# Performance work log

Hardware: AMD Instinct MI355X
Metric: run time of the kernel (lower is better)

The kernel has to match this reference:

```python
import jax, jax.numpy as jnp
import numpy as np

HEADS = 12
D_MODEL = 768
D_K = D_MODEL // HEADS


def setup_inputs() -> dict:
    key = jax.random.key(0)
    ks = jax.random.split(key, 5)
    B, S = 2, 2048
    scale = 1.0 / np.sqrt(D_MODEL)
    return {
        "q": jax.random.normal(ks[0], (B, S, D_MODEL), dtype=jnp.float32),
        "k": jax.random.normal(ks[1], (B, S, D_MODEL), dtype=jnp.float32),
        "v": jax.random.normal(ks[2], (B, S, D_MODEL), dtype=jnp.float32),
        "Wk": jax.random.normal(ks[3], (D_MODEL, D_MODEL), dtype=jnp.float32) * scale,
        "bk": jnp.zeros((D_MODEL,), dtype=jnp.float32),
        "Wo": jax.random.normal(ks[4], (D_MODEL, D_MODEL), dtype=jnp.float32) * scale,
        "bo": jnp.zeros((D_MODEL,), dtype=jnp.float32),
    }


def reference(q, k, v, Wk, bk, Wo, bo):
    B, S, _ = q.shape
    # NOTE: faithful to source bug: q, k, v ALL projected with k_linear.
    def proj(x):
        y = x @ Wk.T + bk                    # [B,S,D]
        return y.reshape(B, -1, HEADS, D_K).transpose(0, 2, 1, 3)  # [B,H,S,Dk]

    qh, kh, vh = proj(q), proj(k), proj(v)
    scores = jnp.einsum('bhsd,bhtd->bhst', qh, kh) / jnp.sqrt(jnp.float32(D_K))
    attn = jax.nn.softmax(scores, axis=-1)   # dropout is identity in eval
    out = jnp.einsum('bhst,bhtd->bhsd', attn, vh)
    concat = out.transpose(0, 2, 1, 3).reshape(B, -1, D_MODEL)
    return concat @ Wo.T + bo
```

## Files before the change

### kernel.cpp

```cpp
#include <hip/hip_runtime.h>
#include <hip/hip_bf16.h>
#include <stddef.h>

#define HEADS 12
#define DM 768
#define DK 64
#define SEQ 2048
#define NB 2
#define WSZ (DM * DM)
#define QSCALE 0.18033688011112043f

typedef __attribute__((ext_vector_type(8))) short short8;
typedef __attribute__((ext_vector_type(4))) float f32x4;

#define MFMA16(A, B, C) __builtin_amdgcn_mfma_f32_16x16x32_bf16((A), (B), (C), 0, 0, 0)

__device__ __forceinline__ unsigned short f2bf(float x) {
  union { float f; unsigned u; } c;
  c.f = x;
  unsigned r = (c.u + 0x7FFFu + ((c.u >> 16) & 1u)) >> 16;
  return (unsigned short)r;
}
__device__ __forceinline__ float bf2f(unsigned short h) {
  union { float f; unsigned u; } c;
  c.u = ((unsigned)h) << 16;
  return c.f;
}

__device__ __forceinline__ void async16(const void* g, void* l) {
  __builtin_amdgcn_global_load_lds(
      (const __attribute__((address_space(1))) void*)g,
      (__attribute__((address_space(3))) void*)l, 16, 0, 0);
}

__device__ __forceinline__ void splitpk(float a, float b, unsigned& hu, unsigned& lu) {
  union { __hip_bfloat162 v; unsigned u; } c;
  c.v = __float22bfloat162_rn(make_float2(a, b));
  hu = c.u;
  const float ra = a - bf2f((unsigned short)(hu & 0xFFFFu));
  const float rb = b - bf2f((unsigned short)(hu >> 16));
  c.v = __float22bfloat162_rn(make_float2(ra, rb));
  lu = c.u;
}
__device__ __forceinline__ unsigned pk2bf(float a, float b) {
  union { __hip_bfloat162 v; unsigned u; } c;
  c.v = __float22bfloat162_rn(make_float2(a, b));
  return c.u;
}


__global__ __launch_bounds__(256) void prep_split(
    const float* __restrict__ q, const float* __restrict__ k,
    const float* __restrict__ v, const float* __restrict__ Wk,
    const float* __restrict__ Wo, unsigned short* __restrict__ xq,
    unsigned short* __restrict__ xk, unsigned short* __restrict__ xv,
    unsigned short* __restrict__ wkh, unsigned short* __restrict__ wkl,
    unsigned short* __restrict__ woh, unsigned short* __restrict__ wol) {
  __shared__ __align__(16) unsigned short Lh[64 * 136];
  __shared__ __align__(16) unsigned short Ll[64 * 136];
  const int tid = threadIdx.x;
  int id = blockIdx.x;
  const float* S;
  unsigned short *H, *L = nullptr;
  int RT, RT16;
  if (id < 1152) {
    S = (id < 384) ? q : (id < 768) ? k : v;
    H = (id < 384) ? xq : (id < 768) ? xk : xv;
    id = id % 384; RT = 64; RT16 = 256;
  } else if (id < 1224) {
    S = Wk; H = wkh; L = wkl; id -= 1152; RT = 12; RT16 = 48;
  } else {
    S = Wo; H = woh; L = wol; id -= 1224; RT = 12; RT16 = 48;
  }
  const int rb = id % RT, kb = id / RT;
  const int mlane = tid >> 4;
  const int klane = (tid & 15) * 8;

#pragma unroll
  for (int rr = 0; rr < 4; ++rr) {
    const int m = rr * 16 + mlane;
    const float* src = &S[(size_t)(rb * 64 + m) * DM + kb * 128 + klane];
    float a[8];
    *(float4*)&a[0] = *(const float4*)&src[0];
    *(float4*)&a[4] = *(const float4*)&src[4];
    if (L) {
      unsigned hu[4], lu[4];
#pragma unroll
      for (int u = 0; u < 4; ++u) splitpk(a[2 * u], a[2 * u + 1], hu[u], lu[u]);
      *(uint4*)&Lh[m * 136 + klane] = *(uint4*)&hu[0];
      *(uint4*)&Ll[m * 136 + klane] = *(uint4*)&lu[0];
    } else {
      unsigned hu[4];
#pragma unroll
      for (int u = 0; u < 4; ++u) hu[u] = pk2bf(a[2 * u], a[2 * u + 1]);
      *(uint4*)&Lh[m * 136 + klane] = *(uint4*)&hu[0];
    }
  }
  __syncthreads();

  const int t = tid >> 4;
  const int ktp = t >> 2, mtp = t & 3;
  const size_t gt = ((size_t)(kb * 4 + ktp) * RT16 + (rb * 4 + mtp)) * 512;
#pragma unroll
  for (int i = 0; i < 4; ++i) {
    const int c = i * 16 + (tid & 15);
    const int lsrc = (mtp * 16 + (tid & 15)) * 136 + ktp * 32 + i * 8;
    *(uint4*)&H[gt + c * 8] = *(uint4*)&Lh[lsrc];
    if (L) *(uint4*)&L[gt + c * 8] = *(uint4*)&Ll[lsrc];
  }
}

__global__ __launch_bounds__(256, 3) void gemm_proj(
    const unsigned short* __restrict__ Xq, const unsigned short* __restrict__ Xk,
    const unsigned short* __restrict__ Xv, const unsigned short* __restrict__ Bh_,
    const unsigned short* __restrict__ Bl_, const float* __restrict__ bias,
    unsigned short* __restrict__ q_h, unsigned short* __restrict__ q_l,
    unsigned short* __restrict__ k_h, unsigned short* __restrict__ vt_h) {
  __shared__ __align__(16) unsigned short Ash[8 * 512];
  __shared__ __align__(16) unsigned short Bsh[6 * 512];
  __shared__ __align__(16) unsigned short Bsl[6 * 512];

  const int tid = threadIdx.x, z = blockIdx.z;
  const unsigned short* __restrict__ A = (z == 0) ? Xq : (z == 1) ? Xk : Xv;
  const int id = blockIdx.x;
  const int mt0 = (id & 31) * 8, nt0 = (id >> 5) * 6;
  const int lane = tid & 63, wv = tid >> 6;
  const int l15 = lane & 15, quad = lane >> 4;
  const int wm = (wv >> 1) * 4, wn = (wv & 1) * 3;
  const int lx = lane * 8;

  f32x4 acc[4][3];
#pragma unroll
  for (int i = 0; i < 4; ++i)
#pragma unroll
    for (int j = 0; j < 3; ++j) acc[i][j] = (f32x4){0.f, 0.f, 0.f, 0.f};

  for (int kt = 0; kt < 24; ++kt) {
    __syncthreads();
    async16(&A[((size_t)kt * 256 + mt0 + wv) * 512 + lx], &Ash[wv * 512]);
    async16(&A[((size_t)kt * 256 + mt0 + wv + 4) * 512 + lx], &Ash[(wv + 4) * 512]);
    async16(&Bh_[((size_t)kt * 48 + nt0 + wv) * 512 + lx], &Bsh[wv * 512]);
    async16(&Bl_[((size_t)kt * 48 + nt0 + wv) * 512 + lx], &Bsl[wv * 512]);
    if (wv < 2)
      async16(&Bh_[((size_t)kt * 48 + nt0 + 4 + wv) * 512 + lx], &Bsh[(4 + wv) * 512]);
    else
      async16(&Bl_[((size_t)kt * 48 + nt0 + 2 + wv) * 512 + lx], &Bsl[(2 + wv) * 512]);
    __syncthreads();

    short8 bh8[3], bl8[3];
#pragma unroll
    for (int nt = 0; nt < 3; ++nt) {
      bh8[nt] = *(const short8*)&Bsh[(wn + nt) * 512 + lx];
      bl8[nt] = *(const short8*)&Bsl[(wn + nt) * 512 + lx];
    }
#pragma unroll
    for (int mt = 0; mt < 4; ++mt) {
      const short8 ah8 = *(const short8*)&Ash[(wm + mt) * 512 + lx];
#pragma unroll
      for (int nt = 0; nt < 3; ++nt) {
        acc[mt][nt] = MFMA16(ah8, bh8[nt], acc[mt][nt]);
        acc[mt][nt] = MFMA16(ah8, bl8[nt], acc[mt][nt]);
      }
    }
  }

#pragma unroll
  for (int mt = 0; mt < 4; ++mt)
#pragma unroll
    for (int nt = 0; nt < 3; ++nt) {
      const int n = (nt0 + wn + nt) * 16 + l15;
      const float bv = bias[n];
      const int hh = n >> 6, dk = n & 63;
#pragma unroll
      for (int j = 0; j < 4; ++j) {
        const int m = (mt0 + wm + mt) * 16 + quad * 4 + j;
        const int b = m >> 11, t = m & 2047;
        const int bh = b * HEADS + hh;
        if (z == 0) {
          const float y = (acc[mt][nt][j] + bv) * QSCALE;
          const unsigned short yh = f2bf(y);
          const int a = (bh * SEQ + t) * DK + dk;
          q_h[a] = yh;
          q_l[a] = f2bf(y - bf2f(yh));
        } else if (z == 1) {
          const int a = bh * 131072 + (dk >> 5) * 65536 + (t >> 4) * 512 +
                        (((dk & 31) >> 3) * 16 + (t & 15)) * 8 + (dk & 7);
          k_h[a] = f2bf(acc[mt][nt][j] + bv);
        } else {
          const int a = bh * 131072 + (t >> 5) * 2048 + (dk >> 4) * 512 +
                        (((t & 31) >> 3) * 16 + (dk & 15)) * 8 + (t & 7);
          vt_h[a] = f2bf(acc[mt][nt][j] + bv);
        }
      }
    }
}

__global__ __launch_bounds__(256, 2) void gemm_out(
    const unsigned short* __restrict__ Ah_, const unsigned short* __restrict__ Al_,
    const unsigned short* __restrict__ Bh_, const unsigned short* __restrict__ Bl_,
    const float* __restrict__ bias, float* __restrict__ outF) {
  __shared__ __align__(16) unsigned short Ash[4 * 512];
  __shared__ __align__(16) unsigned short Asl[4 * 512];
  __shared__ __align__(16) unsigned short Bsh[6 * 512];
  __shared__ __align__(16) unsigned short Bsl[6 * 512];

  const int tid = threadIdx.x, id = blockIdx.x;
  const int mt0 = (id & 63) * 4, nt0 = (id >> 6) * 6;
  const int lane = tid & 63, wv = tid >> 6;
  const int l15 = lane & 15, quad = lane >> 4;
  const int wm = (wv >> 1) * 2, wn = (wv & 1) * 3;
  const int lx = lane * 8;

  f32x4 acc[2][3];
#pragma unroll
  for (int i = 0; i < 2; ++i)
#pragma unroll
    for (int j = 0; j < 3; ++j) acc[i][j] = (f32x4){0.f, 0.f, 0.f, 0.f};

  for (int kt = 0; kt < 24; ++kt) {
    __syncthreads();
    async16(&Ah_[((size_t)kt * 256 + mt0 + wv) * 512 + lx], &Ash[wv * 512]);
    async16(&Al_[((size_t)kt * 256 + mt0 + wv) * 512 + lx], &Asl[wv * 512]);
    async16(&Bh_[((size_t)kt * 48 + nt0 + wv) * 512 + lx], &Bsh[wv * 512]);
    async16(&Bl_[((size_t)kt * 48 + nt0 + wv) * 512 + lx], &Bsl[wv * 512]);
    if (wv < 2)
      async16(&Bh_[((size_t)kt * 48 + nt0 + 4 + wv) * 512 + lx], &Bsh[(4 + wv) * 512]);
    else
      async16(&Bl_[((size_t)kt * 48 + nt0 + 2 + wv) * 512 + lx], &Bsl[(2 + wv) * 512]);
    __syncthreads();

    short8 bh8[3], bl8[3];
#pragma unroll
    for (int nt = 0; nt < 3; ++nt) {
      bh8[nt] = *(const short8*)&Bsh[(wn + nt) * 512 + lx];
      bl8[nt] = *(const short8*)&Bsl[(wn + nt) * 512 + lx];
    }
#pragma unroll
    for (int mt = 0; mt < 2; ++mt) {
      const short8 ah8 = *(const short8*)&Ash[(wm + mt) * 512 + lx];
      const short8 al8 = *(const short8*)&Asl[(wm + mt) * 512 + lx];
#pragma unroll
      for (int nt = 0; nt < 3; ++nt) {
        acc[mt][nt] = MFMA16(ah8, bh8[nt], acc[mt][nt]);
        acc[mt][nt] = MFMA16(al8, bh8[nt], acc[mt][nt]);
        acc[mt][nt] = MFMA16(ah8, bl8[nt], acc[mt][nt]);
      }
    }
  }

#pragma unroll
  for (int mt = 0; mt < 2; ++mt)
#pragma unroll
    for (int nt = 0; nt < 3; ++nt) {
      const int n = (nt0 + wn + nt) * 16 + l15;
      const float bv = bias[n];
#pragma unroll
      for (int j = 0; j < 4; ++j) {
        const int m = (mt0 + wm + mt) * 16 + quad * 4 + j;
        outF[(size_t)m * DM + n] = acc[mt][nt][j] + bv;
      }
    }
}

__global__ __launch_bounds__(256, 3) void attn_mfma(
    const unsigned short* __restrict__ q_h, const unsigned short* __restrict__ q_l,
    const unsigned short* __restrict__ k_h, const unsigned short* __restrict__ vt_h,
    unsigned short* __restrict__ cch, unsigned short* __restrict__ ccl) {
  __shared__ __align__(16) unsigned short Ks[8 * 512];
  __shared__ __align__(16) unsigned short Vs[8 * 512];
  __shared__ __align__(16) unsigned short Ps[4 * 1024];
  __shared__ float Osh[64 * 68];
  __shared__ float Lred[4][2][16];

  const int tid = threadIdx.x, lane = tid & 63, wv = tid >> 6;
  const int l15 = lane & 15, quad = lane >> 4;
  const int qh = wv & 1, th = wv >> 1;
  const int id = blockIdx.x;
  const int bh = id % 24, q0 = (id / 24) << 6;
  const int lx = lane * 8;

  short8 Qf[2][2][2];
#pragma unroll
  for (int qt = 0; qt < 2; ++qt)
#pragma unroll
    for (int ks = 0; ks < 2; ++ks) {
      const int off =
          (bh * SEQ + q0 + qh * 32 + qt * 16 + l15) * DK + ks * 32 + quad * 8;
      Qf[qt][ks][0] = *(const short8*)&q_h[off];
      Qf[qt][ks][1] = *(const short8*)&q_l[off];
    }

  f32x4 O[2][4];
#pragma unroll
  for (int i = 0; i < 2; ++i)
#pragma unroll
    for (int j = 0; j < 4; ++j) O[i][j] = (f32x4){0.f, 0.f, 0.f, 0.f};
  float lsum[2] = {0.f, 0.f};

  const size_t kbase = (size_t)bh * 131072;
  const size_t vbase = (size_t)bh * 131072;

  for (int t0 = 0; t0 < SEQ; t0 += 64) {
    __syncthreads();
    async16(&k_h[kbase + ((size_t)(t0 >> 4) + wv) * 512 + lx], &Ks[wv * 512]);
    async16(&k_h[kbase + 65536 + ((size_t)(t0 >> 4) + wv) * 512 + lx],
            &Ks[(4 + wv) * 512]);
    async16(&vt_h[vbase + (size_t)(t0 >> 5) * 2048 + wv * 512 + lx],
            &Vs[wv * 512]);
    async16(&vt_h[vbase + ((size_t)(t0 >> 5) + 1) * 2048 + wv * 512 + lx],
            &Vs[(4 + wv) * 512]);
    __syncthreads();

    f32x4 St[2][2];
#pragma unroll
    for (int i = 0; i < 2; ++i)
#pragma unroll
      for (int j = 0; j < 2; ++j) St[i][j] = (f32x4){0.f, 0.f, 0.f, 0.f};
#pragma unroll
    for (int ks = 0; ks < 2; ++ks)
#pragma unroll
      for (int tt = 0; tt < 2; ++tt) {
        const short8 kh8 = *(const short8*)&Ks[(ks * 4 + th * 2 + tt) * 512 + lx];
#pragma unroll
        for (int qt = 0; qt < 2; ++qt) {
          St[tt][qt] = MFMA16(kh8, Qf[qt][ks][0], St[tt][qt]);
          St[tt][qt] = MFMA16(kh8, Qf[qt][ks][1], St[tt][qt]);
        }
      }

#pragma unroll
    for (int tt = 0; tt < 2; ++tt)
#pragma unroll
      for (int qt = 0; qt < 2; ++qt) {
        const float p0 = __builtin_amdgcn_exp2f(fminf(St[tt][qt][0], 40.f));
        const float p1 = __builtin_amdgcn_exp2f(fminf(St[tt][qt][1], 40.f));
        const float p2 = __builtin_amdgcn_exp2f(fminf(St[tt][qt][2], 40.f));
        const float p3 = __builtin_amdgcn_exp2f(fminf(St[tt][qt][3], 40.f));
        lsum[qt] += (p0 + p1) + (p2 + p3);
        unsigned pk[2];
        pk[0] = pk2bf(p0, p1);
        pk[1] = pk2bf(p2, p3);
        *(uint2*)&Ps[wv * 1024 + qt * 512 +
                     ((2 * tt + (quad >> 1)) * 16 + l15) * 8 + (quad & 1) * 4] =
            *(uint2*)&pk[0];
      }
    asm volatile("s_waitcnt lgkmcnt(0)" ::: "memory");

    short8 pf[2];
#pragma unroll
    for (int qt = 0; qt < 2; ++qt)
      pf[qt] = *(const short8*)&Ps[wv * 1024 + qt * 512 + lx];
#pragma unroll
    for (int nt = 0; nt < 4; ++nt) {
      const short8 vh8 = *(const short8*)&Vs[(th * 4 + nt) * 512 + lx];
      O[0][nt] = MFMA16(pf[0], vh8, O[0][nt]);
      O[1][nt] = MFMA16(pf[1], vh8, O[1][nt]);
    }
  }

#pragma unroll
  for (int qt = 0; qt < 2; ++qt) {
    float l = lsum[qt];
    l += __shfl_xor(l, 16);
    l += __shfl_xor(l, 32);
    if (quad == 0) Lred[wv][qt][l15] = l;
  }
  __syncthreads();
  if (th == 1) {
#pragma unroll
    for (int qt = 0; qt < 2; ++qt)
#pragma unroll
      for (int nt = 0; nt < 4; ++nt)
#pragma unroll
        for (int j = 0; j < 4; ++j)
          Osh[(qh * 32 + qt * 16 + quad * 4 + j) * 68 + nt * 16 + l15] =
              O[qt][nt][j];
  }
  __syncthreads();
  if (th == 0) {
    const int b = bh / HEADS, hh = bh % HEADS;
#pragma unroll
    for (int qt = 0; qt < 2; ++qt)
#pragma unroll
      for (int j = 0; j < 4; ++j) {
        const int qloc = qh * 32 + qt * 16 + quad * 4 + j;
        const float inv = 1.0f / (Lred[wv][qt][quad * 4 + j] +
                                  Lred[wv + 2][qt][quad * 4 + j]);
        const int m = b * SEQ + q0 + qloc;
#pragma unroll
        for (int nt = 0; nt < 4; ++nt) {
          const float y = (O[qt][nt][j] + Osh[qloc * 68 + nt * 16 + l15]) * inv;
          const int kk = hh * 64 + nt * 16 + l15;
          const int a = ((kk >> 5) * 256 + (m >> 4)) * 512 +
                        (((kk & 31) >> 3) * 16 + (m & 15)) * 8 + (kk & 7);
          const unsigned short yh = f2bf(y);
          cch[a] = yh;
          ccl[a] = f2bf(y - bf2f(yh));
        }
      }
  }
}

extern "C" void kernel_launch(void* const* d_in, const int* in_sizes, int n_in,
                              void* d_out, int out_size, void* d_ws,
                              size_t ws_size, hipStream_t stream) {
  const float* q = (const float*)d_in[0];
  const float* k = (const float*)d_in[1];
  const float* v = (const float*)d_in[2];
  const float* Wk = (const float*)d_in[3];
  const float* bk = (const float*)d_in[4];
  const float* Wo = (const float*)d_in[5];
  const float* bo = (const float*)d_in[6];
  float* out = (float*)d_out;

  const size_t SZ = (size_t)NB * SEQ * DM;
  unsigned short* ws16 = (unsigned short*)d_ws;
  unsigned short* xq = ws16;
  unsigned short* xk = ws16 + SZ;
  unsigned short* xv = ws16 + 2 * SZ;
  unsigned short* cch = xq;
  unsigned short* ccl = xk;
  unsigned short* qp_h = ws16 + 3 * SZ;
  unsigned short* qp_l = ws16 + 4 * SZ;
  unsigned short* kp = ws16 + 5 * SZ;
  unsigned short* vtp = ws16 + 6 * SZ;
  unsigned short* wkh = ws16 + 7 * SZ;
  unsigned short* wkl = wkh + WSZ;
  unsigned short* woh = wkl + WSZ;
  unsigned short* wol = woh + WSZ;

  prep_split<<<dim3(1296), 256, 0, stream>>>(q, k, v, Wk, Wo, xq, xk, xv, wkh,
                                             wkl, woh, wol);
  gemm_proj<<<dim3(256, 1, 3), 256, 0, stream>>>(xq, xk, xv, wkh, wkl, bk,
                                                 qp_h, qp_l, kp, vtp);
  attn_mfma<<<dim3(768), 256, 0, stream>>>(qp_h, qp_l, kp, vtp, cch, ccl);
  gemm_out<<<dim3(512), 256, 0, stream>>>(cch, ccl, woh, wol, bo, out);
}
```

Before: 206.0 us.

## Halve attention query tile to 32 rows and alias LDS buffers for occupancy

```diff
diff --git a/kernel.cpp b/kernel.cpp
--- a/kernel.cpp
+++ b/kernel.cpp
@@ -262,40 +262,37 @@
     }
 }
 
-__global__ __launch_bounds__(256, 3) void attn_mfma(
+__global__ __launch_bounds__(256, 6) void attn_mfma(
     const unsigned short* __restrict__ q_h, const unsigned short* __restrict__ q_l,
     const unsigned short* __restrict__ k_h, const unsigned short* __restrict__ vt_h,
     unsigned short* __restrict__ cch, unsigned short* __restrict__ ccl) {
-  __shared__ __align__(16) unsigned short Ks[8 * 512];
-  __shared__ __align__(16) unsigned short Vs[8 * 512];
-  __shared__ __align__(16) unsigned short Ps[4 * 1024];
-  __shared__ float Osh[64 * 68];
-  __shared__ float Lred[4][2][16];
+  __shared__ __align__(16) unsigned char pool[16384];
+  unsigned short* const Ks = (unsigned short*)pool;
+  unsigned short* const Vs = (unsigned short*)(pool + 8192);
+  float* const Osh = (float*)pool;
+  __shared__ __align__(16) unsigned short Ps[4 * 512];
+  __shared__ float Lred[4][16];
 
   const int tid = threadIdx.x, lane = tid & 63, wv = tid >> 6;
   const int l15 = lane & 15, quad = lane >> 4;
   const int qh = wv & 1, th = wv >> 1;
   const int id = blockIdx.x;
-  const int bh = id % 24, q0 = (id / 24) << 6;
+  const int bh = id % 24, q0 = (id / 24) << 5;
   const int lx = lane * 8;
 
-  short8 Qf[2][2][2];
-#pragma unroll
-  for (int qt = 0; qt < 2; ++qt)
-#pragma unroll
-    for (int ks = 0; ks < 2; ++ks) {
-      const int off =
-          (bh * SEQ + q0 + qh * 32 + qt * 16 + l15) * DK + ks * 32 + quad * 8;
-      Qf[qt][ks][0] = *(const short8*)&q_h[off];
-      Qf[qt][ks][1] = *(const short8*)&q_l[off];
-    }
-
-  f32x4 O[2][4];
-#pragma unroll
-  for (int i = 0; i < 2; ++i)
-#pragma unroll
-    for (int j = 0; j < 4; ++j) O[i][j] = (f32x4){0.f, 0.f, 0.f, 0.f};
-  float lsum[2] = {0.f, 0.f};
+  short8 Qf[2][2];
+#pragma unroll
+  for (int ks = 0; ks < 2; ++ks) {
+    const int off =
+        (bh * SEQ + q0 + qh * 16 + l15) * DK + ks * 32 + quad * 8;
+    Qf[ks][0] = *(const short8*)&q_h[off];
+    Qf[ks][1] = *(const short8*)&q_l[off];
+  }
+
+  f32x4 O[4];
+#pragma unroll
+  for (int j = 0; j < 4; ++j) O[j] = (f32x4){0.f, 0.f, 0.f, 0.f};
+  float lsum = 0.f;
 
   const size_t kbase = (size_t)bh * 131072;
   const size_t vbase = (size_t)bh * 131072;
@@ -311,93 +308,74 @@
             &Vs[(4 + wv) * 512]);
     __syncthreads();
 
-    f32x4 St[2][2];
-#pragma unroll
-    for (int i = 0; i < 2; ++i)
-#pragma unroll
-      for (int j = 0; j < 2; ++j) St[i][j] = (f32x4){0.f, 0.f, 0.f, 0.f};
+    f32x4 St[2];
+#pragma unroll
+    for (int i = 0; i < 2; ++i) St[i] = (f32x4){0.f, 0.f, 0.f, 0.f};
 #pragma unroll
     for (int ks = 0; ks < 2; ++ks)
 #pragma unroll
       for (int tt = 0; tt < 2; ++tt) {
         const short8 kh8 = *(const short8*)&Ks[(ks * 4 + th * 2 + tt) * 512 + lx];
-#pragma unroll
-        for (int qt = 0; qt < 2; ++qt) {
-          St[tt][qt] = MFMA16(kh8, Qf[qt][ks][0], St[tt][qt]);
-          St[tt][qt] = MFMA16(kh8, Qf[qt][ks][1], St[tt][qt]);
-        }
-      }
-
-#pragma unroll
-    for (int tt = 0; tt < 2; ++tt)
-#pragma unroll
-      for (int qt = 0; qt < 2; ++qt) {
-        const float p0 = __builtin_amdgcn_exp2f(fminf(St[tt][qt][0], 40.f));
-        const float p1 = __builtin_amdgcn_exp2f(fminf(St[tt][qt][1], 40.f));
-        const float p2 = __builtin_amdgcn_exp2f(fminf(St[tt][qt][2], 40.f));
-        const float p3 = __builtin_amdgcn_exp2f(fminf(St[tt][qt][3], 40.f));
-        lsum[qt] += (p0 + p1) + (p2 + p3);
-        unsigned pk[2];
-        pk[0] = pk2bf(p0, p1);
-        pk[1] = pk2bf(p2, p3);
-        *(uint2*)&Ps[wv * 1024 + qt * 512 +
-                     ((2 * tt + (quad >> 1)) * 16 + l15) * 8 + (quad & 1) * 4] =
-            *(uint2*)&pk[0];
-      }
+        St[tt] = MFMA16(kh8, Qf[ks][0], St[tt]);
+        St[tt] = MFMA16(kh8, Qf[ks][1], St[tt]);
+      }
+
+#pragma unroll
+    for (int tt = 0; tt < 2; ++tt) {
+      const float p0 = __builtin_amdgcn_exp2f(fminf(St[tt][0], 40.f));
+      const float p1 = __builtin_amdgcn_exp2f(fminf(St[tt][1], 40.f));
+      const float p2 = __builtin_amdgcn_exp2f(fminf(St[tt][2], 40.f));
+      const float p3 = __builtin_amdgcn_exp2f(fminf(St[tt][3], 40.f));
+      lsum += (p0 + p1) + (p2 + p3);
+      unsigned pk[2];
+      pk[0] = pk2bf(p0, p1);
+      pk[1] = pk2bf(p2, p3);
+      *(uint2*)&Ps[wv * 512 +
+                   ((2 * tt + (quad >> 1)) * 16 + l15) * 8 + (quad & 1) * 4] =
+          *(uint2*)&pk[0];
+    }
     asm volatile("s_waitcnt lgkmcnt(0)" ::: "memory");
 
-    short8 pf[2];
-#pragma unroll
-    for (int qt = 0; qt < 2; ++qt)
-      pf[qt] = *(const short8*)&Ps[wv * 1024 + qt * 512 + lx];
+    const short8 pf = *(const short8*)&Ps[wv * 512 + lx];
 #pragma unroll
     for (int nt = 0; nt < 4; ++nt) {
       const short8 vh8 = *(const short8*)&Vs[(th * 4 + nt) * 512 + lx];
-      O[0][nt] = MFMA16(pf[0], vh8, O[0][nt]);
-      O[1][nt] = MFMA16(pf[1], vh8, O[1][nt]);
-    }
-  }
-
-#pragma unroll
-  for (int qt = 0; qt < 2; ++qt) {
-    float l = lsum[qt];
-    l += __shfl_xor(l, 16);
-    l += __shfl_xor(l, 32);
-    if (quad == 0) Lred[wv][qt][l15] = l;
-  }
+      O[nt] = MFMA16(pf, vh8, O[nt]);
+    }
+  }
+
+  float l = lsum;
+  l += __shfl_xor(l, 16);
+  l += __shfl_xor(l, 32);
+  if (quad == 0) Lred[wv][l15] = l;
   __syncthreads();
   if (th == 1) {
 #pragma unroll
-    for (int qt = 0; qt < 2; ++qt)
-#pragma unroll
-      for (int nt = 0; nt < 4; ++nt)
-#pragma unroll
-        for (int j = 0; j < 4; ++j)
-          Osh[(qh * 32 + qt * 16 + quad * 4 + j) * 68 + nt * 16 + l15] =
-              O[qt][nt][j];
+    for (int nt = 0; nt < 4; ++nt)
+#pragma unroll
+      for (int j = 0; j < 4; ++j)
+        Osh[(qh * 16 + quad * 4 + j) * 68 + nt * 16 + l15] = O[nt][j];
   }
   __syncthreads();
   if (th == 0) {
     const int b = bh / HEADS, hh = bh % HEADS;
 #pragma unroll
-    for (int qt = 0; qt < 2; ++qt)
-#pragma unroll
-      for (int j = 0; j < 4; ++j) {
-        const int qloc = qh * 32 + qt * 16 + quad * 4 + j;
-        const float inv = 1.0f / (Lred[wv][qt][quad * 4 + j] +
-                                  Lred[wv + 2][qt][quad * 4 + j]);
-        const int m = b * SEQ + q0 + qloc;
-#pragma unroll
-        for (int nt = 0; nt < 4; ++nt) {
-          const float y = (O[qt][nt][j] + Osh[qloc * 68 + nt * 16 + l15]) * inv;
-          const int kk = hh * 64 + nt * 16 + l15;
-          const int a = ((kk >> 5) * 256 + (m >> 4)) * 512 +
-                        (((kk & 31) >> 3) * 16 + (m & 15)) * 8 + (kk & 7);
-          const unsigned short yh = f2bf(y);
-          cch[a] = yh;
-          ccl[a] = f2bf(y - bf2f(yh));
-        }
-      }
+    for (int j = 0; j < 4; ++j) {
+      const int qloc = qh * 16 + quad * 4 + j;
+      const float inv = 1.0f / (Lred[wv][quad * 4 + j] +
+                                Lred[wv + 2][quad * 4 + j]);
+      const int m = b * SEQ + q0 + qloc;
+#pragma unroll
+      for (int nt = 0; nt < 4; ++nt) {
+        const float y = (O[nt][j] + Osh[qloc * 68 + nt * 16 + l15]) * inv;
+        const int kk = hh * 64 + nt * 16 + l15;
+        const int a = ((kk >> 5) * 256 + (m >> 4)) * 512 +
+                      (((kk & 31) >> 3) * 16 + (m & 15)) * 8 + (kk & 7);
+        const unsigned short yh = f2bf(y);
+        cch[a] = yh;
+        ccl[a] = f2bf(y - bf2f(yh));
+      }
+    }
   }
 }
 
@@ -433,6 +411,6 @@
                                              wkl, woh, wol);
   gemm_proj<<<dim3(256, 1, 3), 256, 0, stream>>>(xq, xk, xv, wkh, wkl, bk,
                                                  qp_h, qp_l, kp, vtp);
-  attn_mfma<<<dim3(768), 256, 0, stream>>>(qp_h, qp_l, kp, vtp, cch, ccl);
+  attn_mfma<<<dim3(1536), 256, 0, stream>>>(qp_h, qp_l, kp, vtp, cch, ccl);
   gemm_out<<<dim3(512), 256, 0, stream>>>(cch, ccl, woh, wol, bo, out);
 }
```

Measured after the change: 207.8 us. About the same (+0.9%).
